# Kernel optimization log

Measured on AMD Instinct MI355X. Metric: run time of the kernel, lower is better.

Reference implementation:

```python
import jax, jax.numpy as jnp
import numpy as np

IOU_POS = 0.5
IOU_NEG = 0.3


def _pairwise_iou(b1, b2):
    # b1: [N,4], b2: [M,4] in xyxy -> [N,M]
    area1 = (b1[:, 2] - b1[:, 0]) * (b1[:, 3] - b1[:, 1])
    area2 = (b2[:, 2] - b2[:, 0]) * (b2[:, 3] - b2[:, 1])
    lt = jnp.maximum(b1[:, None, :2], b2[None, :, :2])
    rb = jnp.minimum(b1[:, None, 2:], b2[None, :, 2:])
    wh = jnp.clip(rb - lt, 0.0)
    inter = wh[..., 0] * wh[..., 1]
    union = area1[:, None] + area2[None, :] - inter
    return inter / jnp.maximum(union, 1e-8)


def _smooth_l1(x):
    ax = jnp.abs(x)
    return jnp.where(ax < 1.0, 0.5 * x * x, ax - 0.5)


def _per_image(cls_o, reg_o, tb, tl):
    # cls_o: [N,C], reg_o: [N,4], tb: [M,4], tl: [M]
    ious = _pairwise_iou(reg_o, tb)            # [N,M]
    max_ious = ious.max(axis=1)
    max_idx = ious.argmax(axis=1)
    pos = max_ious >= IOU_POS
    neg = max_ious < IOU_NEG
    logp = jax.nn.log_softmax(cls_o, axis=-1)  # [N,C]
    matched_lbl = tl[max_idx]                  # [N]
    ce_pos = -jnp.take_along_axis(logp, matched_lbl[:, None], axis=1)[:, 0]
    ce_neg = -logp[:, 0]                       # background class 0
    npos = pos.sum().astype(logp.dtype)
    nneg = neg.sum().astype(logp.dtype)
    cls_loss_pos = jnp.sum(jnp.where(pos, ce_pos, 0.0)) / jnp.maximum(npos, 1.0)
    cls_loss_neg = jnp.sum(jnp.where(neg, ce_neg, 0.0)) / jnp.maximum(nneg, 1.0)
    diff = reg_o - tb[max_idx]                 # [N,4]
    sl1 = _smooth_l1(diff).mean(axis=-1)       # per-anchor mean over 4 coords
    reg_loss = jnp.sum(jnp.where(pos, sl1, 0.0)) / jnp.maximum(npos, 1.0)
    return cls_loss_pos, cls_loss_neg, reg_loss, npos > 0, nneg > 0


def _detection_loss(cls_output, reg_output, target_boxes, target_labels):
    cp, cn, rl, has_p, has_n = jax.vmap(_per_image)(cls_output, reg_output, target_boxes, target_labels)
    cls_vals = jnp.concatenate([cp, cn])
    cls_valid = jnp.concatenate([has_p, has_n]).astype(cls_vals.dtype)
    n_cls = cls_valid.sum()
    cls_mean = jnp.sum(cls_vals * cls_valid) / jnp.maximum(n_cls, 1.0)
    has_pf = has_p.astype(rl.dtype)
    n_reg = has_pf.sum()
    reg_mean = jnp.sum(rl * has_pf) / jnp.maximum(n_reg, 1.0)
    total = jnp.where(n_cls > 0, cls_mean, 0.0) + jnp.where(n_reg > 0, reg_mean, 0.0)
    return total


def setup_inputs() -> dict:
    key = jax.random.key(0)
    k1, k2, k3, k4, k5, k6 = jax.random.split(key, 6)
    B, N, C, M = 8, 131072, 21, 32
    cls_output = jax.random.normal(k1, (B, N, C), dtype=jnp.float32)
    xy = jax.random.uniform(k2, (B, N, 2), minval=0.0, maxval=220.0)
    wh = jax.random.uniform(k3, (B, N, 2), minval=20.0, maxval=80.0)
    reg_output = jnp.concatenate([xy, xy + wh], axis=-1)
    txy = jax.random.uniform(k4, (B, M, 2), minval=0.0, maxval=220.0)
    twh = jax.random.uniform(k5, (B, M, 2), minval=20.0, maxval=80.0)
    target_boxes = jnp.concatenate([txy, txy + twh], axis=-1)
    target_labels = jax.random.randint(k6, (B, M), 1, C)
    return {"cls_output": cls_output, "reg_output": reg_output,
            "target_boxes": target_boxes, "target_labels": target_labels}


def reference(cls_output, reg_output, target_boxes, target_labels):
    return _detection_loss(cls_output, reg_output, target_boxes, target_labels)
```

## Files before the change

kernel.cpp:

```cpp
#include <hip/hip_runtime.h>
#include <math.h>

#define TPB 256
#define NC 21
#define NM 32

__global__ __launch_bounds__(256) void detloss_prep(
    const float* __restrict__ tbx, float* __restrict__ prep, int total)
{
    const int i = blockIdx.x * blockDim.x + threadIdx.x;
    if (i < total) {
        const float4 tb = ((const float4*)tbx)[i];
        float* q = prep + i * 8;
        q[0] = tb.x; q[1] = tb.y; q[2] = tb.z; q[3] = tb.w;
        q[4] = (tb.z - tb.x) * (tb.w - tb.y);
        q[5] = 0.f; q[6] = 0.f; q[7] = 0.f;
    }
}

__global__ __launch_bounds__(TPB) void detloss_main(
    const float* __restrict__ cls, const float* __restrict__ reg,
    const float* __restrict__ tbx, const int* __restrict__ tlb,
    const float* __restrict__ prep, float* __restrict__ partials,
    int N, int nblk)
{
    __shared__ float s_red[TPB / 64][5];

    const int t    = threadIdx.x;
    const int lane = t & 63;
    const int w    = t >> 6;
    const int blk  = blockIdx.x;
    const int b    = blockIdx.y;
    const int row  = blk * TPB + t;
    const int rowi = (row < N) ? row : (N - 1);
    const float msk = (row < N) ? 1.f : 0.f;

    const float4 rg = ((const float4*)reg)[(size_t)b * N + rowi];
    const float a1 = (rg.z - rg.x) * (rg.w - rg.y);

    const char* xg = (const char*)(cls + ((size_t)b * N + rowi) * NC);
    float4 c0, c1, c2, c3, c4; float c5;
    __builtin_memcpy(&c0, xg,      16);
    __builtin_memcpy(&c1, xg + 16, 16);
    __builtin_memcpy(&c2, xg + 32, 16);
    __builtin_memcpy(&c3, xg + 48, 16);
    __builtin_memcpy(&c4, xg + 64, 16);
    __builtin_memcpy(&c5, xg + 80, 4);

    const float* __restrict__ tp = prep + (size_t)b * NM * 8;
    unsigned kbest = 0u;
    #pragma unroll
    for (int j = 0; j < NM; ++j) {
        const float tx = tp[j * 8 + 0], ty = tp[j * 8 + 1];
        const float tz = tp[j * 8 + 2], tw = tp[j * 8 + 3];
        const float ta = tp[j * 8 + 4];
        const float lx = fmaxf(rg.x, tx), ly = fmaxf(rg.y, ty);
        const float rx = fminf(rg.z, tz), ry = fminf(rg.w, tw);
        const float wd = fmaxf(rx - lx, 0.f), h = fmaxf(ry - ly, 0.f);
        const float inter = wd * h;
        const float uni   = (a1 + ta) - inter;
        const float iou   = inter * __builtin_amdgcn_rcpf(uni);
        const unsigned key = (__float_as_uint(iou) & 0xFFFFFFE0u)
                           | (unsigned)(31 - j);
        kbest = (key > kbest) ? key : kbest;
    }
    const int   bidx = 31 - (int)(kbest & 31u);
    const float best = __uint_as_float(kbest & 0xFFFFFFE0u);
    const bool  pos  = (best >= 0.5f);
    const bool  neg  = (best <  0.3f);

    const int    lbl = tlb[b * NM + bidx];
    const float4 mb  = ((const float4*)tbx)[b * NM + bidx];
    float xlbl;
    __builtin_memcpy(&xlbl, xg + 4 * lbl, 4);

    float s0 = __expf(c0.x) + __expf(c0.y) + __expf(c0.z) + __expf(c0.w);
    float s1 = __expf(c1.x) + __expf(c1.y) + __expf(c1.z) + __expf(c1.w);
    float s2 = __expf(c2.x) + __expf(c2.y) + __expf(c2.z) + __expf(c2.w);
    float s3 = __expf(c3.x) + __expf(c3.y) + __expf(c3.z) + __expf(c3.w);
    s0 += __expf(c4.x) + __expf(c4.y);
    s1 += __expf(c4.z) + __expf(c4.w);
    s2 += __expf(c5);
    const float lse    = __logf((s0 + s1) + (s2 + s3));
    const float ce_pos = lse - xlbl;
    const float ce_neg = lse - c0.x;

    float sl = 0.f;
    {
        const float d0 = rg.x - mb.x, d1 = rg.y - mb.y;
        const float d2 = rg.z - mb.z, d3 = rg.w - mb.w;
        const float e0 = fabsf(d0), e1 = fabsf(d1);
        const float e2 = fabsf(d2), e3 = fabsf(d3);
        sl += (e0 < 1.f) ? 0.5f * d0 * d0 : (e0 - 0.5f);
        sl += (e1 < 1.f) ? 0.5f * d1 * d1 : (e1 - 0.5f);
        sl += (e2 < 1.f) ? 0.5f * d2 * d2 : (e2 - 0.5f);
        sl += (e3 < 1.f) ? 0.5f * d3 * d3 : (e3 - 0.5f);
        sl *= 0.25f;
    }

    const float pm = (pos ? 1.f : 0.f) * msk;
    const float nm = (neg ? 1.f : 0.f) * msk;
    float v0 = pm * ce_pos, v2 = pm * sl, v3 = pm;
    float v1 = nm * ce_neg, v4 = nm;

    #pragma unroll
    for (int o = 32; o > 0; o >>= 1) {
        v0 += __shfl_down(v0, o);
        v1 += __shfl_down(v1, o);
        v2 += __shfl_down(v2, o);
        v3 += __shfl_down(v3, o);
        v4 += __shfl_down(v4, o);
    }
    if (lane == 0) {
        s_red[w][0] = v0; s_red[w][1] = v1; s_red[w][2] = v2;
        s_red[w][3] = v3; s_red[w][4] = v4;
    }
    __syncthreads();
    if (t == 0) {
        float r0 = 0, r1 = 0, r2 = 0, r3 = 0, r4 = 0;
        #pragma unroll
        for (int k = 0; k < TPB / 64; ++k) {
            r0 += s_red[k][0]; r1 += s_red[k][1]; r2 += s_red[k][2];
            r3 += s_red[k][3]; r4 += s_red[k][4];
        }
        float* q = partials + ((size_t)b * nblk + blk) * 5;
        q[0] = r0; q[1] = r1; q[2] = r2; q[3] = r3; q[4] = r4;
    }
}

__global__ __launch_bounds__(512) void detloss_final(
    const float* __restrict__ partials, int nblk, int B, float* __restrict__ out)
{
    __shared__ float s_img[8][5];
    const int t    = threadIdx.x;
    const int b    = t >> 6;
    const int lane = t & 63;

    if (b < B) {
        float v[5] = {0.f, 0.f, 0.f, 0.f, 0.f};
        for (int e = lane; e < nblk; e += 64) {
            const float* q = partials + ((size_t)b * nblk + e) * 5;
            #pragma unroll
            for (int k = 0; k < 5; ++k) v[k] += q[k];
        }
        #pragma unroll
        for (int o = 32; o > 0; o >>= 1) {
            #pragma unroll
            for (int k = 0; k < 5; ++k) v[k] += __shfl_down(v[k], o);
        }
        if (lane == 0) {
            const float npos = v[3], nneg = v[4];
            s_img[b][0] = v[0] / fmaxf(npos, 1.f);
            s_img[b][1] = v[1] / fmaxf(nneg, 1.f);
            s_img[b][2] = v[2] / fmaxf(npos, 1.f);
            s_img[b][3] = (npos > 0.f) ? 1.f : 0.f;
            s_img[b][4] = (nneg > 0.f) ? 1.f : 0.f;
        }
    }
    __syncthreads();

    if (t == 0) {
        float cls_sum = 0.f, n_cls = 0.f, reg_sum = 0.f, n_reg = 0.f;
        for (int b2 = 0; b2 < B; ++b2) {
            cls_sum += s_img[b2][0] * s_img[b2][3] + s_img[b2][1] * s_img[b2][4];
            n_cls   += s_img[b2][3] + s_img[b2][4];
            reg_sum += s_img[b2][2] * s_img[b2][3];
            n_reg   += s_img[b2][3];
        }
        const float cls_mean = cls_sum / fmaxf(n_cls, 1.f);
        const float reg_mean = reg_sum / fmaxf(n_reg, 1.f);
        out[0] = ((n_cls > 0.f) ? cls_mean : 0.f) + ((n_reg > 0.f) ? reg_mean : 0.f);
    }
}

extern "C" void kernel_launch(void* const* d_in, const int* in_sizes, int n_in,
                              void* d_out, int out_size, void* d_ws, size_t ws_size,
                              hipStream_t stream) {
    const float* cls = (const float*)d_in[0];
    const float* reg = (const float*)d_in[1];
    const float* tbx = (const float*)d_in[2];
    const int*   tlb = (const int*)d_in[3];
    float*       out = (float*)d_out;

    float* ws       = (float*)d_ws;
    float* prep     = ws;
    float* partials = ws + 2048;

    const int B = 8;
    const int N = in_sizes[1] / (B * 4);
    const int nblk = (N + TPB - 1) / TPB;

    detloss_prep<<<1, 256, 0, stream>>>(tbx, prep, B * NM);
    dim3 grid(nblk, B);
    detloss_main<<<grid, TPB, 0, stream>>>(cls, reg, tbx, tlb, prep, partials, N, nblk);
    detloss_final<<<1, 512, 0, stream>>>(partials, nblk, B, out);
}
```

Before: 37.36 us.

## Drop prep kernel and process four row tiles per block

Removes the separate target-box prep kernel and computes target box areas inline from the raw boxes inside the IoU loop. Each block now loops over four 256-row tiles and accumulates its partial sums in registers, which cuts the grid size, the number of partial records and the work of the final reduction by four. This saves one kernel launch and reduces reduction overhead. The cost is more redundant area arithmetic per anchor, fewer blocks in flight, and no overlap between tiles inside a thread, since the loop is not unrolled.

```diff
diff --git a/kernel.cpp b/kernel.cpp
--- a/kernel.cpp
+++ b/kernel.cpp
@@ -2,27 +2,14 @@
 #include <math.h>
 
 #define TPB 256
+#define TPB4 4
 #define NC 21
 #define NM 32
-
-__global__ __launch_bounds__(256) void detloss_prep(
-    const float* __restrict__ tbx, float* __restrict__ prep, int total)
-{
-    const int i = blockIdx.x * blockDim.x + threadIdx.x;
-    if (i < total) {
-        const float4 tb = ((const float4*)tbx)[i];
-        float* q = prep + i * 8;
-        q[0] = tb.x; q[1] = tb.y; q[2] = tb.z; q[3] = tb.w;
-        q[4] = (tb.z - tb.x) * (tb.w - tb.y);
-        q[5] = 0.f; q[6] = 0.f; q[7] = 0.f;
-    }
-}
 
 __global__ __launch_bounds__(TPB) void detloss_main(
     const float* __restrict__ cls, const float* __restrict__ reg,
     const float* __restrict__ tbx, const int* __restrict__ tlb,
-    const float* __restrict__ prep, float* __restrict__ partials,
-    int N, int nblk)
+    float* __restrict__ partials, int N, int gxb)
 {
     __shared__ float s_red[TPB / 64][5];
 
@@ -31,77 +18,83 @@
     const int w    = t >> 6;
     const int blk  = blockIdx.x;
     const int b    = blockIdx.y;
-    const int row  = blk * TPB + t;
-    const int rowi = (row < N) ? row : (N - 1);
-    const float msk = (row < N) ? 1.f : 0.f;
+    const int ntiles = (N + TPB - 1) / TPB;
+    const int tile0  = blk * TPB4;
+    const int tile1  = min(tile0 + TPB4, ntiles);
 
-    const float4 rg = ((const float4*)reg)[(size_t)b * N + rowi];
-    const float a1 = (rg.z - rg.x) * (rg.w - rg.y);
+    float v0 = 0.f, v1 = 0.f, v2 = 0.f, v3 = 0.f, v4 = 0.f;
 
-    const char* xg = (const char*)(cls + ((size_t)b * N + rowi) * NC);
-    float4 c0, c1, c2, c3, c4; float c5;
-    __builtin_memcpy(&c0, xg,      16);
-    __builtin_memcpy(&c1, xg + 16, 16);
-    __builtin_memcpy(&c2, xg + 32, 16);
-    __builtin_memcpy(&c3, xg + 48, 16);
-    __builtin_memcpy(&c4, xg + 64, 16);
-    __builtin_memcpy(&c5, xg + 80, 4);
+    for (int tile = tile0; tile < tile1; ++tile) {
+        const int row  = tile * TPB + t;
+        const int rowi = (row < N) ? row : (N - 1);
+        const float msk = (row < N) ? 1.f : 0.f;
 
-    const float* __restrict__ tp = prep + (size_t)b * NM * 8;
-    unsigned kbest = 0u;
-    #pragma unroll
-    for (int j = 0; j < NM; ++j) {
-        const float tx = tp[j * 8 + 0], ty = tp[j * 8 + 1];
-        const float tz = tp[j * 8 + 2], tw = tp[j * 8 + 3];
-        const float ta = tp[j * 8 + 4];
-        const float lx = fmaxf(rg.x, tx), ly = fmaxf(rg.y, ty);
-        const float rx = fminf(rg.z, tz), ry = fminf(rg.w, tw);
-        const float wd = fmaxf(rx - lx, 0.f), h = fmaxf(ry - ly, 0.f);
-        const float inter = wd * h;
-        const float uni   = (a1 + ta) - inter;
-        const float iou   = inter * __builtin_amdgcn_rcpf(uni);
-        const unsigned key = (__float_as_uint(iou) & 0xFFFFFFE0u)
-                           | (unsigned)(31 - j);
-        kbest = (key > kbest) ? key : kbest;
+        const float4 rg = ((const float4*)reg)[(size_t)b * N + rowi];
+        const float a1 = (rg.z - rg.x) * (rg.w - rg.y);
+
+        const char* xg = (const char*)(cls + ((size_t)b * N + rowi) * NC);
+        float4 c0, c1, c2, c3, c4; float c5;
+        __builtin_memcpy(&c0, xg,      16);
+        __builtin_memcpy(&c1, xg + 16, 16);
+        __builtin_memcpy(&c2, xg + 32, 16);
+        __builtin_memcpy(&c3, xg + 48, 16);
+        __builtin_memcpy(&c4, xg + 64, 16);
+        __builtin_memcpy(&c5, xg + 80, 4);
+
+        unsigned kbest = 0u;
+        #pragma unroll
+        for (int j = 0; j < NM; ++j) {
+            const float4 tb = ((const float4*)tbx)[b * NM + j];
+            const float ta = (tb.z - tb.x) * (tb.w - tb.y);
+            const float lx = fmaxf(rg.x, tb.x), ly = fmaxf(rg.y, tb.y);
+            const float rx = fminf(rg.z, tb.z), ry = fminf(rg.w, tb.w);
+            const float wd = fmaxf(rx - lx, 0.f), h = fmaxf(ry - ly, 0.f);
+            const float inter = wd * h;
+            const float uni   = (a1 + ta) - inter;
+            const float iou   = inter * __builtin_amdgcn_rcpf(uni);
+            const unsigned key = (__float_as_uint(iou) & 0xFFFFFFE0u)
+                               | (unsigned)(31 - j);
+            kbest = (key > kbest) ? key : kbest;
+        }
+        const int   bidx = 31 - (int)(kbest & 31u);
+        const float best = __uint_as_float(kbest & 0xFFFFFFE0u);
+        const bool  pos  = (best >= 0.5f);
+        const bool  neg  = (best <  0.3f);
+
+        const int    lbl = tlb[b * NM + bidx];
+        const float4 mb  = ((const float4*)tbx)[b * NM + bidx];
+        float xlbl;
+        __builtin_memcpy(&xlbl, xg + 4 * lbl, 4);
+
+        float s0 = __expf(c0.x) + __expf(c0.y) + __expf(c0.z) + __expf(c0.w);
+        float s1 = __expf(c1.x) + __expf(c1.y) + __expf(c1.z) + __expf(c1.w);
+        float s2 = __expf(c2.x) + __expf(c2.y) + __expf(c2.z) + __expf(c2.w);
+        float s3 = __expf(c3.x) + __expf(c3.y) + __expf(c3.z) + __expf(c3.w);
+        s0 += __expf(c4.x) + __expf(c4.y);
+        s1 += __expf(c4.z) + __expf(c4.w);
+        s2 += __expf(c5);
+        const float lse    = __logf((s0 + s1) + (s2 + s3));
+        const float ce_pos = lse - xlbl;
+        const float ce_neg = lse - c0.x;
+
+        float sl = 0.f;
+        {
+            const float d0 = rg.x - mb.x, d1 = rg.y - mb.y;
+            const float d2 = rg.z - mb.z, d3 = rg.w - mb.w;
+            const float e0 = fabsf(d0), e1 = fabsf(d1);
+            const float e2 = fabsf(d2), e3 = fabsf(d3);
+            sl += (e0 < 1.f) ? 0.5f * d0 * d0 : (e0 - 0.5f);
+            sl += (e1 < 1.f) ? 0.5f * d1 * d1 : (e1 - 0.5f);
+            sl += (e2 < 1.f) ? 0.5f * d2 * d2 : (e2 - 0.5f);
+            sl += (e3 < 1.f) ? 0.5f * d3 * d3 : (e3 - 0.5f);
+            sl *= 0.25f;
+        }
+
+        const float pm = (pos ? 1.f : 0.f) * msk;
+        const float nm = (neg ? 1.f : 0.f) * msk;
+        v0 += pm * ce_pos; v2 += pm * sl; v3 += pm;
+        v1 += nm * ce_neg; v4 += nm;
     }
-    const int   bidx = 31 - (int)(kbest & 31u);
-    const float best = __uint_as_float(kbest & 0xFFFFFFE0u);
-    const bool  pos  = (best >= 0.5f);
-    const bool  neg  = (best <  0.3f);
-
-    const int    lbl = tlb[b * NM + bidx];
-    const float4 mb  = ((const float4*)tbx)[b * NM + bidx];
-    float xlbl;
-    __builtin_memcpy(&xlbl, xg + 4 * lbl, 4);
-
-    float s0 = __expf(c0.x) + __expf(c0.y) + __expf(c0.z) + __expf(c0.w);
-    float s1 = __expf(c1.x) + __expf(c1.y) + __expf(c1.z) + __expf(c1.w);
-    float s2 = __expf(c2.x) + __expf(c2.y) + __expf(c2.z) + __expf(c2.w);
-    float s3 = __expf(c3.x) + __expf(c3.y) + __expf(c3.z) + __expf(c3.w);
-    s0 += __expf(c4.x) + __expf(c4.y);
-    s1 += __expf(c4.z) + __expf(c4.w);
-    s2 += __expf(c5);
-    const float lse    = __logf((s0 + s1) + (s2 + s3));
-    const float ce_pos = lse - xlbl;
-    const float ce_neg = lse - c0.x;
-
-    float sl = 0.f;
-    {
-        const float d0 = rg.x - mb.x, d1 = rg.y - mb.y;
-        const float d2 = rg.z - mb.z, d3 = rg.w - mb.w;
-        const float e0 = fabsf(d0), e1 = fabsf(d1);
-        const float e2 = fabsf(d2), e3 = fabsf(d3);
-        sl += (e0 < 1.f) ? 0.5f * d0 * d0 : (e0 - 0.5f);
-        sl += (e1 < 1.f) ? 0.5f * d1 * d1 : (e1 - 0.5f);
-        sl += (e2 < 1.f) ? 0.5f * d2 * d2 : (e2 - 0.5f);
-        sl += (e3 < 1.f) ? 0.5f * d3 * d3 : (e3 - 0.5f);
-        sl *= 0.25f;
-    }
-
-    const float pm = (pos ? 1.f : 0.f) * msk;
-    const float nm = (neg ? 1.f : 0.f) * msk;
-    float v0 = pm * ce_pos, v2 = pm * sl, v3 = pm;
-    float v1 = nm * ce_neg, v4 = nm;
 
     #pragma unroll
     for (int o = 32; o > 0; o >>= 1) {
@@ -123,7 +116,7 @@
             r0 += s_red[k][0]; r1 += s_red[k][1]; r2 += s_red[k][2];
             r3 += s_red[k][3]; r4 += s_red[k][4];
         }
-        float* q = partials + ((size_t)b * nblk + blk) * 5;
+        float* q = partials + ((size_t)b * gxb + blk) * 5;
         q[0] = r0; q[1] = r1; q[2] = r2; q[3] = r3; q[4] = r4;
     }
 }
@@ -181,17 +174,14 @@
     const float* tbx = (const float*)d_in[2];
     const int*   tlb = (const int*)d_in[3];
     float*       out = (float*)d_out;
-
-    float* ws       = (float*)d_ws;
-    float* prep     = ws;
-    float* partials = ws + 2048;
+    float*  partials = (float*)d_ws;
 
     const int B = 8;
     const int N = in_sizes[1] / (B * 4);
-    const int nblk = (N + TPB - 1) / TPB;
+    const int ntiles = (N + TPB - 1) / TPB;
+    const int gxb    = (ntiles + TPB4 - 1) / TPB4;
 
-    detloss_prep<<<1, 256, 0, stream>>>(tbx, prep, B * NM);
-    dim3 grid(nblk, B);
-    detloss_main<<<grid, TPB, 0, stream>>>(cls, reg, tbx, tlb, prep, partials, N, nblk);
-    detloss_final<<<1, 512, 0, stream>>>(partials, nblk, B, out);
+    dim3 grid(gxb, B);
+    detloss_main<<<grid, TPB, 0, stream>>>(cls, reg, tbx, tlb, partials, N, gxb);
+    detloss_final<<<1, 512, 0, stream>>>(partials, gxb, B, out);
 }
```

New measurement: 40.74 us. 9.1% more time.
